# Performance work log

Hardware: AMD Instinct MI355X
Metric: run time of the kernel (lower is better)

Reference implementation:

```python
import jax, jax.numpy as jnp
import numpy as np

D = 256
NR_PATHS, PATH_LEN = 4096, 64
NR_NODES = 10000


def setup_inputs() -> dict:
    key = jax.random.key(0)
    ks = jax.random.split(key, 6)
    encoded_paths = jax.random.normal(ks[0], (NR_PATHS, PATH_LEN, D), dtype=jnp.float32)
    paths_mask = jax.random.randint(ks[1], (NR_PATHS, PATH_LEN), 0, 2).astype(jnp.bool_)
    paths_node_indices = jax.random.randint(ks[2], (NR_PATHS, PATH_LEN), 0, NR_NODES)
    previous_nodes_encodings = jax.random.normal(ks[3], (NR_NODES, D), dtype=jnp.float32)
    Wq = jax.random.normal(ks[4], (D, D), dtype=jnp.float32) / np.sqrt(D)
    gate_W = jax.random.normal(ks[5], (2 * D, D), dtype=jnp.float32) / np.sqrt(2 * D)
    gate_b = jnp.zeros((D,), dtype=jnp.float32)
    return {
        'encoded_paths': encoded_paths,
        'paths_mask': paths_mask,
        'paths_node_indices': paths_node_indices,
        'previous_nodes_encodings': previous_nodes_encodings,
        'Wq': Wq,
        'gate_W': gate_W,
        'gate_b': gate_b,
        'nr_nodes': NR_NODES,
    }


def _scatter_attn_combine(x, idx, m, queries, Wq, nr_nodes):
    # x: [N, D] flattened path-step encodings; idx: [N] target node; m: [N] bool mask
    d = x.shape[-1]
    q = queries @ Wq                                   # [nodes, D] attention queries
    scores = jnp.einsum('nd,nd->n', q[idx], x) / jnp.sqrt(jnp.asarray(d, x.dtype))
    scores = jnp.where(m, scores, jnp.asarray(-1e30, x.dtype))
    seg_max = jax.ops.segment_max(scores, idx, num_segments=nr_nodes)
    seg_max = jnp.where(jnp.isfinite(seg_max), seg_max, jnp.zeros_like(seg_max))
    e = jnp.exp(scores - seg_max[idx]) * m.astype(x.dtype)
    denom = jax.ops.segment_sum(e, idx, num_segments=nr_nodes)
    probs = e / jnp.maximum(denom[idx], jnp.asarray(1e-9, x.dtype))
    return jax.ops.segment_sum(probs[:, None] * x, idx, num_segments=nr_nodes)


def reference(encoded_paths, paths_mask, paths_node_indices,
              previous_nodes_encodings, Wq, gate_W, gate_b, nr_nodes):
    d = encoded_paths.shape[-1]
    x = encoded_paths.reshape(-1, d)
    idx = paths_node_indices.reshape(-1)
    m = paths_mask.reshape(-1)
    # attention-weighted scatter of masked path-step encodings onto nodes
    update = _scatter_attn_combine(x, idx, m, previous_nodes_encodings, Wq, nr_nodes)
    # gated state update: g = sigmoid([prev; update] W + b); new = g*prev + (1-g)*update
    g = jax.nn.sigmoid(jnp.concatenate([previous_nodes_encodings, update], axis=-1) @ gate_W + gate_b)
    return g * previous_nodes_encodings + (1.0 - g) * update
```

## Files before the change

kernel.cpp:

```cpp
#include <hip/hip_runtime.h>

#define D 256
#define NPATHS 4096
#define PLEN 64
#define NSTEPS (NPATHS * PLEN)
#define NNODES 10000

__global__ __launch_bounds__(256) void k_query(const float* __restrict__ prev,
                                               const float* __restrict__ Wq,
                                               float* __restrict__ q) {
    __shared__ float a[32][D];
    const int tid = threadIdx.x;
    const int row0 = blockIdx.x * 32;
    for (int i = tid; i < 32 * D; i += 256) {
        int r = i >> 8, c = i & 255;
        int row = row0 + r;
        a[r][c] = (row < NNODES) ? prev[row * D + c] : 0.f;
    }
    __syncthreads();
    float acc[32];
#pragma unroll
    for (int r = 0; r < 32; ++r) acc[r] = 0.f;
    for (int k = 0; k < D; k += 4) {
        float w0 = Wq[(k + 0) * D + tid];
        float w1 = Wq[(k + 1) * D + tid];
        float w2 = Wq[(k + 2) * D + tid];
        float w3 = Wq[(k + 3) * D + tid];
#pragma unroll
        for (int r = 0; r < 32; ++r) {
            float4 av = *reinterpret_cast<const float4*>(&a[r][k]);
            acc[r] += av.x * w0 + av.y * w1 + av.z * w2 + av.w * w3;
        }
    }
    for (int r = 0; r < 32; ++r) {
        int row = row0 + r;
        if (row < NNODES) q[row * D + tid] = acc[r];
    }
}

__global__ __launch_bounds__(256) void k_scores(const float* __restrict__ x,
                                                const int* __restrict__ mask,
                                                const int* __restrict__ nidx,
                                                const float* __restrict__ q,
                                                float* __restrict__ scores,
                                                int* __restrict__ counts) {
    const int wave = threadIdx.x >> 6;
    const int lane = threadIdx.x & 63;
    const int step = blockIdx.x * 4 + wave;
    if (step >= NSTEPS) return;
    if (!mask[step]) return;
    const int node = nidx[step];
    const float4* x4 = reinterpret_cast<const float4*>(x) + step * 64;
    const float4* q4 = reinterpret_cast<const float4*>(q) + node * 64;
    float4 xa = x4[lane];
    float4 qa = q4[lane];
    float v = xa.x * qa.x + xa.y * qa.y + xa.z * qa.z + xa.w * qa.w;
    v += __shfl_down(v, 32);
    v += __shfl_down(v, 16);
    v += __shfl_down(v, 8);
    v += __shfl_down(v, 4);
    v += __shfl_down(v, 2);
    v += __shfl_down(v, 1);
    if (lane == 0) {
        scores[step] = v * 0.0625f;
        atomicAdd(&counts[node], 1);
    }
}

__global__ __launch_bounds__(256) void k_scan(const int* __restrict__ counts,
                                              int* __restrict__ offsets,
                                              int* __restrict__ cursor) {
    __shared__ int sums[256];
    __shared__ int scan[257];
    const int tid = threadIdx.x;
    const int CH = 40;
    const int base = tid * CH;
    int s = 0;
    for (int i = 0; i < CH; ++i) {
        int j = base + i;
        if (j < NNODES) s += counts[j];
    }
    sums[tid] = s;
    __syncthreads();
    if (tid == 0) {
        int run = 0;
        for (int t = 0; t < 256; ++t) { scan[t] = run; run += sums[t]; }
        scan[256] = run;
    }
    __syncthreads();
    int run = scan[tid];
    for (int i = 0; i < CH; ++i) {
        int j = base + i;
        if (j < NNODES) {
            offsets[j] = run;
            cursor[j] = run;
            run += counts[j];
        }
    }
    if (tid == 0) offsets[NNODES] = scan[256];
}

__global__ __launch_bounds__(256) void k_perm(const int* __restrict__ mask,
                                              const int* __restrict__ nidx,
                                              int* __restrict__ cursor,
                                              int* __restrict__ perm) {
    const int step = blockIdx.x * 256 + threadIdx.x;
    if (step >= NSTEPS) return;
    if (!mask[step]) return;
    const int node = nidx[step];
    int p = atomicAdd(&cursor[node], 1);
    perm[p] = step;
}

__global__ __launch_bounds__(256) void k_combine(const float* __restrict__ x,
                                                 const float* __restrict__ scores,
                                                 const int* __restrict__ offsets,
                                                 const int* __restrict__ perm,
                                                 float* __restrict__ update) {
    const int node = blockIdx.x;
    const int tid = threadIdx.x;
    const int off = offsets[node];
    const int cnt = offsets[node + 1] - off;
    if (cnt == 0) {
        update[node * D + tid] = 0.f;
        return;
    }
    __shared__ float red[256];
    __shared__ float smax_s, denom_s;
    float lm = -3.0e38f;
    for (int i = tid; i < cnt; i += 256) lm = fmaxf(lm, scores[perm[off + i]]);
    red[tid] = lm;
    __syncthreads();
    for (int s = 128; s > 0; s >>= 1) {
        if (tid < s) red[tid] = fmaxf(red[tid], red[tid + s]);
        __syncthreads();
    }
    if (tid == 0) smax_s = red[0];
    __syncthreads();
    const float smax = smax_s;
    float ls = 0.f;
    for (int i = tid; i < cnt; i += 256) ls += expf(scores[perm[off + i]] - smax);
    __syncthreads();
    red[tid] = ls;
    __syncthreads();
    for (int s = 128; s > 0; s >>= 1) {
        if (tid < s) red[tid] += red[tid + s];
        __syncthreads();
    }
    if (tid == 0) denom_s = red[0];
    __syncthreads();
    const float invD = 1.f / fmaxf(denom_s, 1e-9f);
    __shared__ int ids[64];
    __shared__ float wts[64];
    float acc = 0.f;
    for (int base = 0; base < cnt; base += 64) {
        if (tid < 64 && base + tid < cnt) {
            int n = perm[off + base + tid];
            ids[tid] = n;
            wts[tid] = expf(scores[n] - smax) * invD;
        }
        __syncthreads();
        int lim = min(64, cnt - base);
        for (int i = 0; i < lim; ++i) {
            acc += wts[i] * x[(size_t)ids[i] * D + tid];
        }
        __syncthreads();
    }
    update[node * D + tid] = acc;
}

__global__ __launch_bounds__(256) void k_gate(const float* __restrict__ prev,
                                              const float* __restrict__ update,
                                              const float* __restrict__ gW,
                                              const float* __restrict__ gb,
                                              float* __restrict__ out) {
    __shared__ float pa[16][D];
    __shared__ float ua[16][D];
    const int tid = threadIdx.x;
    const int row0 = blockIdx.x * 16;
    for (int i = tid; i < 16 * D; i += 256) {
        int r = i >> 8, c = i & 255;
        int row = row0 + r;
        pa[r][c] = (row < NNODES) ? prev[row * D + c] : 0.f;
        ua[r][c] = (row < NNODES) ? update[row * D + c] : 0.f;
    }
    __syncthreads();
    float acc[16];
#pragma unroll
    for (int r = 0; r < 16; ++r) acc[r] = 0.f;
    for (int k = 0; k < D; k += 4) {
        float w0 = gW[(k + 0) * D + tid];
        float w1 = gW[(k + 1) * D + tid];
        float w2 = gW[(k + 2) * D + tid];
        float w3 = gW[(k + 3) * D + tid];
#pragma unroll
        for (int r = 0; r < 16; ++r) {
            float4 av = *reinterpret_cast<const float4*>(&pa[r][k]);
            acc[r] += av.x * w0 + av.y * w1 + av.z * w2 + av.w * w3;
        }
    }
    for (int k = 0; k < D; k += 4) {
        float w0 = gW[(256 + k + 0) * D + tid];
        float w1 = gW[(256 + k + 1) * D + tid];
        float w2 = gW[(256 + k + 2) * D + tid];
        float w3 = gW[(256 + k + 3) * D + tid];
#pragma unroll
        for (int r = 0; r < 16; ++r) {
            float4 av = *reinterpret_cast<const float4*>(&ua[r][k]);
            acc[r] += av.x * w0 + av.y * w1 + av.z * w2 + av.w * w3;
        }
    }
    const float b = gb[tid];
    for (int r = 0; r < 16; ++r) {
        int row = row0 + r;
        if (row < NNODES) {
            float g = 1.f / (1.f + expf(-(acc[r] + b)));
            out[row * D + tid] = g * pa[r][tid] + (1.f - g) * ua[r][tid];
        }
    }
}

extern "C" void kernel_launch(void* const* d_in, const int* in_sizes, int n_in,
                              void* d_out, int out_size, void* d_ws, size_t ws_size,
                              hipStream_t stream) {
    const float* enc   = (const float*)d_in[0];
    const int*   mask  = (const int*)d_in[1];
    const int*   nidx  = (const int*)d_in[2];
    const float* prev  = (const float*)d_in[3];
    const float* Wq    = (const float*)d_in[4];
    const float* gW    = (const float*)d_in[5];
    const float* gb    = (const float*)d_in[6];
    float* out = (float*)d_out;

    char* ws = (char*)d_ws;
    float* q       = (float*)(ws + 0);
    float* scores  = (float*)(ws + 10240000);
    int*   counts  = (int*)  (ws + 11288576);
    int*   offsets = (int*)  (ws + 11328768);
    int*   cursor  = (int*)  (ws + 11369216);
    int*   perm    = (int*)  (ws + 11409408);
    float* update  = (float*)(ws + 12457984);

    hipMemsetAsync(counts, 0, NNODES * sizeof(int), stream);

    k_query<<<(NNODES + 31) / 32, 256, 0, stream>>>(prev, Wq, q);
    k_scores<<<NSTEPS / 4, 256, 0, stream>>>(enc, mask, nidx, q, scores, counts);
    k_scan<<<1, 256, 0, stream>>>(counts, offsets, cursor);
    k_perm<<<NSTEPS / 256, 256, 0, stream>>>(mask, nidx, cursor, perm);
    k_combine<<<NNODES, 256, 0, stream>>>(enc, scores, offsets, perm, update);
    k_gate<<<(NNODES + 15) / 16, 256, 0, stream>>>(prev, update, gW, gb, out);
}
```

Baseline: 608.8 us.

## Fuse score computation into combine with online softmax, one wave per node

The separate score kernel that read every masked path encoding is replaced by a lightweight count kernel. The combine kernel now computes each score from the gathered row and folds it into an online-softmax accumulator, one wave per node, with a one-step prefetch of the next row. This removes one full pass over the ~268MB encoding tensor and the block-wide reductions, at the cost of a serial per-node loop that may be less latency-tolerant for high-degree nodes.

New measurement: 584.9 us. 3.9% less time.

```diff
diff --git a/kernel.cpp b/kernel.cpp
--- a/kernel.cpp
+++ b/kernel.cpp
@@ -38,33 +38,13 @@
     }
 }
 
-__global__ __launch_bounds__(256) void k_scores(const float* __restrict__ x,
-                                                const int* __restrict__ mask,
-                                                const int* __restrict__ nidx,
-                                                const float* __restrict__ q,
-                                                float* __restrict__ scores,
-                                                int* __restrict__ counts) {
-    const int wave = threadIdx.x >> 6;
-    const int lane = threadIdx.x & 63;
-    const int step = blockIdx.x * 4 + wave;
+__global__ __launch_bounds__(256) void k_count(const int* __restrict__ mask,
+                                               const int* __restrict__ nidx,
+                                               int* __restrict__ counts) {
+    const int step = blockIdx.x * 256 + threadIdx.x;
     if (step >= NSTEPS) return;
     if (!mask[step]) return;
-    const int node = nidx[step];
-    const float4* x4 = reinterpret_cast<const float4*>(x) + step * 64;
-    const float4* q4 = reinterpret_cast<const float4*>(q) + node * 64;
-    float4 xa = x4[lane];
-    float4 qa = q4[lane];
-    float v = xa.x * qa.x + xa.y * qa.y + xa.z * qa.z + xa.w * qa.w;
-    v += __shfl_down(v, 32);
-    v += __shfl_down(v, 16);
-    v += __shfl_down(v, 8);
-    v += __shfl_down(v, 4);
-    v += __shfl_down(v, 2);
-    v += __shfl_down(v, 1);
-    if (lane == 0) {
-        scores[step] = v * 0.0625f;
-        atomicAdd(&counts[node], 1);
-    }
+    atomicAdd(&counts[nidx[step]], 1);
 }
 
 __global__ __launch_bounds__(256) void k_scan(const int* __restrict__ counts,
@@ -113,60 +93,59 @@
 }
 
 __global__ __launch_bounds__(256) void k_combine(const float* __restrict__ x,
-                                                 const float* __restrict__ scores,
+                                                 const float* __restrict__ q,
                                                  const int* __restrict__ offsets,
                                                  const int* __restrict__ perm,
                                                  float* __restrict__ update) {
-    const int node = blockIdx.x;
-    const int tid = threadIdx.x;
+    const int wave = threadIdx.x >> 6;
+    const int lane = threadIdx.x & 63;
+    const int node = blockIdx.x * 4 + wave;
+    if (node >= NNODES) return;
     const int off = offsets[node];
     const int cnt = offsets[node + 1] - off;
-    if (cnt == 0) {
-        update[node * D + tid] = 0.f;
-        return;
-    }
-    __shared__ float red[256];
-    __shared__ float smax_s, denom_s;
-    float lm = -3.0e38f;
-    for (int i = tid; i < cnt; i += 256) lm = fmaxf(lm, scores[perm[off + i]]);
-    red[tid] = lm;
-    __syncthreads();
-    for (int s = 128; s > 0; s >>= 1) {
-        if (tid < s) red[tid] = fmaxf(red[tid], red[tid + s]);
-        __syncthreads();
-    }
-    if (tid == 0) smax_s = red[0];
-    __syncthreads();
-    const float smax = smax_s;
-    float ls = 0.f;
-    for (int i = tid; i < cnt; i += 256) ls += expf(scores[perm[off + i]] - smax);
-    __syncthreads();
-    red[tid] = ls;
-    __syncthreads();
-    for (int s = 128; s > 0; s >>= 1) {
-        if (tid < s) red[tid] += red[tid + s];
-        __syncthreads();
-    }
-    if (tid == 0) denom_s = red[0];
-    __syncthreads();
-    const float invD = 1.f / fmaxf(denom_s, 1e-9f);
-    __shared__ int ids[64];
-    __shared__ float wts[64];
-    float acc = 0.f;
-    for (int base = 0; base < cnt; base += 64) {
-        if (tid < 64 && base + tid < cnt) {
-            int n = perm[off + base + tid];
-            ids[tid] = n;
-            wts[tid] = expf(scores[n] - smax) * invD;
-        }
-        __syncthreads();
-        int lim = min(64, cnt - base);
-        for (int i = 0; i < lim; ++i) {
-            acc += wts[i] * x[(size_t)ids[i] * D + tid];
-        }
-        __syncthreads();
-    }
-    update[node * D + tid] = acc;
+
+    const float4* x4 = reinterpret_cast<const float4*>(x);
+    float4 qa = reinterpret_cast<const float4*>(q)[(size_t)node * 64 + lane];
+
+    float4 acc = make_float4(0.f, 0.f, 0.f, 0.f);
+    float m = -3.0e38f;
+    float l = 0.f;
+
+    int step = (cnt > 0) ? perm[off] : 0;
+    float4 xa = (cnt > 0) ? x4[(size_t)step * 64 + lane]
+                          : make_float4(0.f, 0.f, 0.f, 0.f);
+
+    for (int i = 0; i < cnt; ++i) {
+        int step_n = 0;
+        if (i + 1 < cnt) step_n = perm[off + i + 1];
+        float4 xn = make_float4(0.f, 0.f, 0.f, 0.f);
+        if (i + 1 < cnt) xn = x4[(size_t)step_n * 64 + lane];
+
+        float s = xa.x * qa.x + xa.y * qa.y + xa.z * qa.z + xa.w * qa.w;
+        s += __shfl_xor(s, 32);
+        s += __shfl_xor(s, 16);
+        s += __shfl_xor(s, 8);
+        s += __shfl_xor(s, 4);
+        s += __shfl_xor(s, 2);
+        s += __shfl_xor(s, 1);
+        s *= 0.0625f;
+
+        float mn = fmaxf(m, s);
+        float scale = __expf(m - mn);
+        float w = __expf(s - mn);
+        l = l * scale + w;
+        acc.x = acc.x * scale + w * xa.x;
+        acc.y = acc.y * scale + w * xa.y;
+        acc.z = acc.z * scale + w * xa.z;
+        acc.w = acc.w * scale + w * xa.w;
+        m = mn;
+
+        xa = xn;
+    }
+
+    const float inv = 1.f / fmaxf(l, 1e-9f);
+    float4 o = make_float4(acc.x * inv, acc.y * inv, acc.z * inv, acc.w * inv);
+    reinterpret_cast<float4*>(update)[(size_t)node * 64 + lane] = o;
 }
 
 __global__ __launch_bounds__(256) void k_gate(const float* __restrict__ prev,
@@ -234,19 +213,18 @@
 
     char* ws = (char*)d_ws;
     float* q       = (float*)(ws + 0);
-    float* scores  = (float*)(ws + 10240000);
-    int*   counts  = (int*)  (ws + 11288576);
-    int*   offsets = (int*)  (ws + 11328768);
-    int*   cursor  = (int*)  (ws + 11369216);
-    int*   perm    = (int*)  (ws + 11409408);
-    float* update  = (float*)(ws + 12457984);
+    int*   counts  = (int*)  (ws + 10240000);
+    int*   offsets = (int*)  (ws + 10280192);
+    int*   cursor  = (int*)  (ws + 10320640);
+    int*   perm    = (int*)  (ws + 10360832);
+    float* update  = (float*)(ws + 11409408);
 
     hipMemsetAsync(counts, 0, NNODES * sizeof(int), stream);
 
     k_query<<<(NNODES + 31) / 32, 256, 0, stream>>>(prev, Wq, q);
-    k_scores<<<NSTEPS / 4, 256, 0, stream>>>(enc, mask, nidx, q, scores, counts);
+    k_count<<<NSTEPS / 256, 256, 0, stream>>>(mask, nidx, counts);
     k_scan<<<1, 256, 0, stream>>>(counts, offsets, cursor);
     k_perm<<<NSTEPS / 256, 256, 0, stream>>>(mask, nidx, cursor, perm);
-    k_combine<<<NNODES, 256, 0, stream>>>(enc, scores, offsets, perm, update);
+    k_combine<<<(NNODES + 3) / 4, 256, 0, stream>>>(enc, q, offsets, perm, update);
     k_gate<<<(NNODES + 15) / 16, 256, 0, stream>>>(prev, update, gW, gb, out);
 }
```
